# Kernel tuning notes

Measured on AMD Instinct MI355X. Metric: run time of the kernel, lower is better.

Reference implementation:

```python
import jax, jax.numpy as jnp
import numpy as np

NPOINT, RADIUS, NSAMPLE = 1024, 0.4, 32
BN_EPS = 1e-5


def fps(xyz, npoint):
    # xyz: [B, N, 3]. Deterministic start at index 0 (torch uses randint).
    B, N, _ = xyz.shape

    def step(carry, _):
        distance, farthest = carry  # [B,N], [B]
        centroid = jnp.take_along_axis(xyz, farthest[:, None, None], axis=1)  # [B,1,3]
        dist = jnp.sum((xyz - centroid) ** 2, -1)  # [B,N]
        distance = jnp.minimum(distance, dist)
        new_far = jnp.argmax(distance, axis=-1).astype(jnp.int32)
        return (distance, new_far), farthest

    init = (jnp.full((B, N), 1e10, xyz.dtype), jnp.zeros((B,), jnp.int32))
    _, cents = jax.lax.scan(step, init, None, length=npoint)  # [npoint, B]
    return cents.T  # [B, npoint]


def square_distance(src, dst):
    # src [B,S,3], dst [B,N,3] -> [B,S,N]
    d = -2.0 * jnp.einsum('bsc,bnc->bsn', src, dst)
    d = d + jnp.sum(src ** 2, -1)[:, :, None] + jnp.sum(dst ** 2, -1)[:, None, :]
    return jnp.clip(d, 1e-12, None)


def query_ball_point(radius, nsample, xyz, new_xyz):
    B, N, _ = xyz.shape
    S = new_xyz.shape[1]
    sqr = square_distance(new_xyz, xyz)  # [B,S,N]
    gi = jnp.where(sqr > radius ** 2, N, jnp.arange(N, dtype=jnp.int32)[None, None, :])
    gi = jnp.sort(gi, axis=-1)[:, :, :nsample]  # [B,S,K]
    first = gi[:, :, :1]
    return jnp.where(gi == N, first, gi)


def gather_points(points, idx):
    # points [B,N,C], idx [B,S,K] -> [B,S,K,C]
    B, S, K = idx.shape
    C = points.shape[-1]
    flat = jnp.take_along_axis(points, idx.reshape(B, S * K)[:, :, None], axis=1)
    return flat.reshape(B, S, K, C)


def setup_inputs() -> dict:
    key = jax.random.key(0)
    ks = jax.random.split(key, 10)
    B, N, D = 8, 4096, 64
    inp = {
        'xyz': jax.random.normal(ks[0], (B, 3, N), jnp.float32),
        'points': jax.random.normal(ks[1], (B, D, N), jnp.float32),
    }
    chans = [67, 64, 64, 128]
    for i in range(3):
        cin, cout = chans[i], chans[i + 1]
        inp[f'W{i}'] = jax.random.normal(ks[2 + i], (cout, cin), jnp.float32) * (1.0 / np.sqrt(cin))
        inp[f'b{i}'] = jnp.zeros((cout,), jnp.float32)
        inp[f'g{i}'] = jnp.ones((cout,), jnp.float32)
        inp[f'bt{i}'] = jnp.zeros((cout,), jnp.float32)
    return inp


def _forward(xyz, points, Ws, bs, gs, bts):
    xyz_t = jnp.transpose(xyz, (0, 2, 1))      # [B,N,3]
    pts_t = jnp.transpose(points, (0, 2, 1))   # [B,N,D]
    B, N, _ = xyz_t.shape

    fps_idx = fps(xyz_t, NPOINT)                              # [B,S]
    new_xyz = jnp.take_along_axis(xyz_t, fps_idx[:, :, None], axis=1)  # [B,S,3]
    idx = query_ball_point(RADIUS, NSAMPLE, xyz_t, new_xyz)   # [B,S,K]

    grouped_xyz = gather_points(xyz_t, idx)                   # [B,S,K,3]
    grouped_xyz_norm = grouped_xyz - new_xyz[:, :, None, :]
    grouped_pts = gather_points(pts_t, idx)                   # [B,S,K,D]
    new_points = jnp.concatenate([grouped_xyz_norm, grouped_pts], -1)  # [B,S,K,3+D]

    x = jnp.transpose(new_points, (0, 3, 2, 1))  # [B,C,K,S]
    for W, b, g, bt in zip(Ws, bs, gs, bts):
        x = jnp.einsum('oc,bcks->boks', W, x) + b[None, :, None, None]
        mean = jnp.mean(x, axis=(0, 2, 3), keepdims=True)
        var = jnp.var(x, axis=(0, 2, 3), keepdims=True)
        x = (x - mean) * jax.lax.rsqrt(var + BN_EPS)
        x = x * g[None, :, None, None] + bt[None, :, None, None]
        x = jax.nn.relu(x)
    out = jnp.max(x, axis=2)                      # [B,C_out,S]
    return jnp.transpose(new_xyz, (0, 2, 1)), out


def reference(xyz, points, W0, b0, g0, bt0, W1, b1, g1, bt1, W2, b2, g2, bt2):
    return _forward(xyz, points, (W0, W1, W2), (b0, b1, b2), (g0, g1, g2), (bt0, bt1, bt2))
```

## Files before the change

### kernel.cpp

```cpp
#include <hip/hip_runtime.h>
#include <cstddef>
#include <cstdint>

#define NB 8
#define NPTS 4096
#define NS 1024
#define NK 32
#define ND 64

typedef __attribute__((ext_vector_type(8))) short bf16x8;
typedef __attribute__((ext_vector_type(4))) float f32x4;

__device__ __forceinline__ short f2bf(float f) {
  unsigned u = __float_as_uint(f);
  u += 0x7FFF + ((u >> 16) & 1);
  return (short)(u >> 16);
}

#define DPP_IMAX(v, ctrl)                                                     \
  {                                                                           \
    int _o = __builtin_amdgcn_update_dpp(v, v, ctrl, 0xf, 0xf, false);        \
    v = (_o > v) ? _o : v;                                                    \
  }

#define DPP_U64MAX(hi, lo, ctrl)                                              \
  {                                                                           \
    unsigned _nh = (unsigned)__builtin_amdgcn_update_dpp((int)(hi), (int)(hi),\
                                                         ctrl, 0xf, 0xf, false);\
    unsigned _nl = (unsigned)__builtin_amdgcn_update_dpp((int)(lo), (int)(lo),\
                                                         ctrl, 0xf, 0xf, false);\
    bool _gt = (_nh > (hi)) || (_nh == (hi) && _nl > (lo));                   \
    hi = _gt ? _nh : (hi);                                                    \
    lo = _gt ? _nl : (lo);                                                    \
  }

#define DPP_FADD(v, ctrl)                                                     \
  {                                                                           \
    int _t = __builtin_amdgcn_update_dpp(__float_as_int(v), __float_as_int(v),\
                                         ctrl, 0xf, 0xf, false);              \
    v = v + __int_as_float(_t);                                               \
  }

#define DPP_RED16(v, OP)                                                      \
  {                                                                           \
    int _i;                                                                   \
    _i = __builtin_amdgcn_update_dpp(__float_as_int(v), __float_as_int(v), 0x111, 0xf, 0xf, false); \
    v = OP(v, __int_as_float(_i));                                            \
    _i = __builtin_amdgcn_update_dpp(__float_as_int(v), __float_as_int(v), 0x112, 0xf, 0xf, false); \
    v = OP(v, __int_as_float(_i));                                            \
    _i = __builtin_amdgcn_update_dpp(__float_as_int(v), __float_as_int(v), 0x114, 0xf, 0xf, false); \
    v = OP(v, __int_as_float(_i));                                            \
    _i = __builtin_amdgcn_update_dpp(__float_as_int(v), __float_as_int(v), 0x118, 0xf, 0xf, false); \
    v = OP(v, __int_as_float(_i));                                            \
  }

__device__ __forceinline__ float fadd_op(float a, float b) { return a + b; }

__global__ __launch_bounds__(512) void fps_pgemm_kernel(
    const float* __restrict__ xyz, float* __restrict__ out_newxyz,
    float* __restrict__ ws_newxyz, const float* __restrict__ points,
    const float* __restrict__ W0, const float* __restrict__ b0g,
    float* __restrict__ P1) {
  __shared__ __align__(16) char smem[53376];
  const int t = threadIdx.x;

  if (blockIdx.x < 8) {
    float* sXYZ = (float*)smem;
    unsigned long long(*sRed)[8] =
        (unsigned long long(*)[8])(smem + 49152);
    int* sWidx = (int*)(smem + 49280);
    const int b = blockIdx.x;
    const int wave = t >> 6;
    const int lane = t & 63;
    const float* xb = xyz + (size_t)b * 3 * NPTS;

    for (int i = t; i < NPTS; i += 512) {
      sXYZ[i * 3 + 0] = xb[i];
      sXYZ[i * 3 + 1] = xb[NPTS + i];
      sXYZ[i * 3 + 2] = xb[2 * NPTS + i];
    }
    if (t == 0) sWidx[0] = 0;

    float px[8], py[8], pz[8], dist[8];
    {
      float4 a0 = ((const float4*)xb)[2 * t];
      float4 a1 = ((const float4*)xb)[2 * t + 1];
      float4 b0v = ((const float4*)(xb + NPTS))[2 * t];
      float4 b1v = ((const float4*)(xb + NPTS))[2 * t + 1];
      float4 c0 = ((const float4*)(xb + 2 * NPTS))[2 * t];
      float4 c1 = ((const float4*)(xb + 2 * NPTS))[2 * t + 1];
      px[0] = a0.x; px[1] = a0.y; px[2] = a0.z; px[3] = a0.w;
      px[4] = a1.x; px[5] = a1.y; px[6] = a1.z; px[7] = a1.w;
      py[0] = b0v.x; py[1] = b0v.y; py[2] = b0v.z; py[3] = b0v.w;
      py[4] = b1v.x; py[5] = b1v.y; py[6] = b1v.z; py[7] = b1v.w;
      pz[0] = c0.x; pz[1] = c0.y; pz[2] = c0.z; pz[3] = c0.w;
      pz[4] = c1.x; pz[5] = c1.y; pz[6] = c1.z; pz[7] = c1.w;
    }
#pragma unroll
    for (int j = 0; j < 8; ++j) dist[j] = 1e10f;

    float cx = xb[0], cy = xb[NPTS], cz = xb[2 * NPTS];

    for (int s = 0; s < NS; ++s) {
#pragma unroll
      for (int j = 0; j < 8; ++j) {
        float dx = __fadd_rn(px[j], -cx);
        float dy = __fadd_rn(py[j], -cy);
        float dz = __fadd_rn(pz[j], -cz);
        float d = __fadd_rn(__fadd_rn(__fmul_rn(dx, dx), __fmul_rn(dy, dy)),
                            __fmul_rn(dz, dz));
        dist[j] = fminf(dist[j], d);
      }
      float m = fmaxf(fmaxf(fmaxf(dist[0], dist[1]), fmaxf(dist[2], dist[3])),
                      fmaxf(fmaxf(dist[4], dist[5]), fmaxf(dist[6], dist[7])));
      int v = __float_as_int(m);
      DPP_IMAX(v, 0x111)
      DPP_IMAX(v, 0x112)
      DPP_IMAX(v, 0x114)
      DPP_IMAX(v, 0x118)
      DPP_IMAX(v, 0x142)
      DPP_IMAX(v, 0x143)
      const int wm_i = __builtin_amdgcn_readlane(v, 63);
      const float wm = __int_as_float(wm_i);
      unsigned long long claim = __ballot(m == wm);
      int firstlane = __ffsll(claim) - 1;
      if (lane == firstlane) {
        int j = 7;
#pragma unroll
        for (int jj = 6; jj >= 0; --jj)
          if (dist[jj] == wm) j = jj;
        unsigned widx = (unsigned)(t * 8 + j);
        sRed[s & 1][wave] = ((unsigned long long)(unsigned)wm_i << 32) |
                            (unsigned long long)(0xFFFFFFFFu - widx);
      }
      __syncthreads();
      unsigned long long k = sRed[s & 1][lane & 7];
      unsigned h2 = (unsigned)(k >> 32), l2 = (unsigned)k;
      DPP_U64MAX(h2, l2, 0x111)
      DPP_U64MAX(h2, l2, 0x112)
      DPP_U64MAX(h2, l2, 0x114)
      const unsigned gl = (unsigned)__builtin_amdgcn_readlane((int)l2, 7);
      const int widx = (int)(0xFFFFFFFFu - gl);
      cx = sXYZ[widx * 3 + 0];
      cy = sXYZ[widx * 3 + 1];
      cz = sXYZ[widx * 3 + 2];
      if (t == 0 && s < NS - 1) sWidx[s + 1] = widx;
    }
    __syncthreads();
    for (int s2 = t; s2 < NS; s2 += 512) {
      int w = sWidx[s2];
      float x = sXYZ[w * 3 + 0], y = sXYZ[w * 3 + 1], z = sXYZ[w * 3 + 2];
      out_newxyz[b * 3 * NS + s2] = x;
      out_newxyz[b * 3 * NS + NS + s2] = y;
      out_newxyz[b * 3 * NS + 2 * NS + s2] = z;
      ws_newxyz[((b << 10) + s2) * 3 + 0] = x;
      ws_newxyz[((b << 10) + s2) * 3 + 1] = y;
      ws_newxyz[((b << 10) + s2) * 3 + 2] = z;
    }
  } else {
    float* sP = (float*)smem;
    float* sW = (float*)(smem + 16384);
    float* sB = (float*)(smem + 33792);
    const int blk = blockIdx.x - 8;
    const int bb = blk >> 6;
    const int n0 = (blk & 63) * 64;
    const float* pb = points + (size_t)bb * ND * NPTS;
    for (int f = t; f < 4096; f += 512) {
      int c = f >> 6, n = f & 63;
      sP[f] = pb[c * NPTS + n0 + n];
    }
    for (int f = t; f < 4096; f += 512) {
      int c = f >> 6, o = f & 63;
      sW[c * 68 + o] = W0[o * 67 + 3 + c];
    }
    if (t < 64) sB[t] = b0g[t];
    __syncthreads();
    if (t < 256) {
      const int nl = (t & 15) * 4;
      const int ol = (t >> 4) * 4;
      float acc[4][4];
#pragma unroll
      for (int i = 0; i < 4; ++i)
#pragma unroll
        for (int j = 0; j < 4; ++j) acc[i][j] = 0.f;
#pragma unroll 4
      for (int c = 0; c < 64; ++c) {
        float4 xv = *(const float4*)(sP + c * 64 + nl);
        float4 wv = *(const float4*)(sW + c * 68 + ol);
        float xa[4] = {xv.x, xv.y, xv.z, xv.w};
        float wa[4] = {wv.x, wv.y, wv.z, wv.w};
#pragma unroll
        for (int i = 0; i < 4; ++i)
#pragma unroll
          for (int j = 0; j < 4; ++j) acc[i][j] += xa[i] * wa[j];
      }
#pragma unroll
      for (int i = 0; i < 4; ++i) {
        float4 v = make_float4(acc[i][0] + sB[ol + 0], acc[i][1] + sB[ol + 1],
                               acc[i][2] + sB[ol + 2], acc[i][3] + sB[ol + 3]);
        *(float4*)(P1 + ((size_t)(bb << 12) + n0 + nl + i) * 64 + ol) = v;
      }
    }
  }
}

__global__ __launch_bounds__(256) void query_gstats_kernel(
    const float* __restrict__ xyz, const float* __restrict__ ws_newxyz,
    const float* __restrict__ P1, const float* __restrict__ W0,
    int* __restrict__ idx_ws, float* __restrict__ partials) {
  const int w = threadIdx.x >> 6;
  const int lane = threadIdx.x & 63;
  const int p = blockIdx.x * 4 + w;
  const int b = p >> 10;
  __shared__ int sIdx[4][32];
  __shared__ float sWS[4][64];
  __shared__ float sWQ[4][64];
  const float* xb = xyz + (size_t)b * 3 * NPTS;
  const float cx = ws_newxyz[p * 3 + 0];
  const float cy = ws_newxyz[p * 3 + 1];
  const float cz = ws_newxyz[p * 3 + 2];
  const float ss = __fadd_rn(__fadd_rn(__fmul_rn(cx, cx), __fmul_rn(cy, cy)), __fmul_rn(cz, cz));
  const float r2 = (float)(0.4 * 0.4);
  int cnt = 0;
  for (int ci = 0; ci < 64 && cnt < 32; ++ci) {
    int n = ci * 64 + lane;
    float x = xb[n], y = xb[NPTS + n], z = xb[2 * NPTS + n];
    float dot = __fadd_rn(__fadd_rn(__fmul_rn(cx, x), __fmul_rn(cy, y)), __fmul_rn(cz, z));
    float dd = __fadd_rn(__fadd_rn(__fmul_rn(x, x), __fmul_rn(y, y)), __fmul_rn(z, z));
    float d = __fmul_rn(-2.0f, dot);
    d = __fadd_rn(d, ss);
    d = __fadd_rn(d, dd);
    d = fmaxf(d, 1e-12f);
    bool inc = (d <= r2);
    unsigned long long m = __ballot(inc);
    int slot = cnt + (int)__popcll(m & ((1ull << lane) - 1ull));
    if (inc && slot < 32) sIdx[w][slot] = n;
    cnt += (int)__popcll(m);
  }
  if (lane < 32) {
    int v;
    if (lane < cnt) v = sIdx[w][lane];
    else v = (cnt > 0) ? sIdx[w][0] : 0;
    idx_ws[p * 32 + lane] = v;
    sIdx[w][lane] = v;
  }
  const float wx = W0[lane * 67 + 0];
  const float wy = W0[lane * 67 + 1];
  const float wz = W0[lane * 67 + 2];
  float ssum = 0.f, ssq = 0.f;
  for (int r = 0; r < 32; ++r) {
    const int n = sIdx[w][r];
    float P1v = P1[((size_t)(b << 12) + n) * 64 + lane];
    float dx = __fadd_rn(xb[n], -cx);
    float dy = __fadd_rn(xb[NPTS + n], -cy);
    float dz = __fadd_rn(xb[2 * NPTS + n], -cz);
    float y = P1v + (dx * wx + dy * wy + dz * wz);
    ssum += y;
    ssq += y * y;
  }
  sWS[w][lane] = ssum;
  sWQ[w][lane] = ssq;
  __syncthreads();
  const int t = threadIdx.x;
  if (t < 64) {
    float s1 = sWS[0][t] + sWS[1][t] + sWS[2][t] + sWS[3][t];
    float s2 = sWQ[0][t] + sWQ[1][t] + sWQ[2][t] + sWQ[3][t];
    partials[(size_t)blockIdx.x * 128 + t] = s1;
    partials[(size_t)blockIdx.x * 128 + 64 + t] = s2;
  }
}

__global__ __launch_bounds__(256) void conv1_kernel(
    const float* __restrict__ xyz, const float* __restrict__ P1,
    const int* __restrict__ idx_ws, const float* __restrict__ cen_ws,
    const float* __restrict__ W0, const float* __restrict__ W1,
    const float* __restrict__ bias, const float* __restrict__ scaleA,
    const float* __restrict__ shiftA, float* __restrict__ y1,
    float* __restrict__ partials) {
  constexpr int CIN = 64, COUT = 64, WP = 68, TPS = 128;
  __shared__ __align__(16) float sW[CIN * WP];
  __shared__ __align__(16) float sX[2 * CIN * 32];
  __shared__ float sY[64 * 65];
  __shared__ int sIdx[64];
  __shared__ float sCen[2 * 4];
  __shared__ float sScale[CIN];
  __shared__ float sShift[CIN];
  __shared__ float sSum[COUT];
  __shared__ float sSq[COUT];

  const int t = threadIdx.x;
  const int wave = t >> 6, lane = t & 63;
  const int pair0 = blockIdx.x * 2;
  const int b = pair0 >> 10;

  for (int f = t; f < CIN * COUT; f += 256) {
    int o = f / CIN;
    int c = f - o * CIN;
    sW[c * WP + o] = W1[f];
  }
  if (t < CIN) { sScale[t] = scaleA[t]; sShift[t] = shiftA[t]; }
  if (t < COUT) { sSum[t] = 0.f; sSq[t] = 0.f; }
  if (t < 64) sIdx[t] = idx_ws[pair0 * 32 + t];
  if (t < 6) sCen[(t / 3) * 4 + (t % 3)] = cen_ws[pair0 * 3 + t];
  const float wx = W0[lane * 67 + 0];
  const float wy = W0[lane * 67 + 1];
  const float wz = W0[lane * 67 + 2];
  __syncthreads();
  const float* xb = xyz + (size_t)b * 3 * NPTS;
  for (int r = wave; r < 64; r += 4) {
    const int sl = r >> 5;
    const int n = sIdx[r];
    float P1v = P1[((size_t)(b << 12) + n) * 64 + lane];
    float dx = __fadd_rn(xb[n], -sCen[sl * 4 + 0]);
    float dy = __fadd_rn(xb[NPTS + n], -sCen[sl * 4 + 1]);
    float dz = __fadd_rn(xb[2 * NPTS + n], -sCen[sl * 4 + 2]);
    sY[r * 65 + lane] = P1v + (dx * wx + dy * wy + dz * wz);
  }
  __syncthreads();
  for (int f = t; f < 2 * CIN * 32; f += 256) {
    int sl = f >> 11;
    int rmd = f & 2047;
    int o = rmd >> 5, k = rmd & 31;
    float v = sY[(sl * 32 + k) * 65 + o];
    v = v * sScale[o] + sShift[o];
    sX[f] = fmaxf(v, 0.f);
  }
  __syncthreads();

  const int sl = t / TPS;
  const int tl = t - sl * TPS;
  const int k0 = (tl & 7) * 4;
  const int o0 = (tl >> 3) * 4;

  float acc[4][4];
#pragma unroll
  for (int i = 0; i < 4; ++i)
#pragma unroll
    for (int j = 0; j < 4; ++j) acc[i][j] = 0.f;

  const float* xrow = sX + sl * (CIN * 32);
#pragma unroll 4
  for (int c = 0; c < CIN; ++c) {
    float4 xv = *(const float4*)(xrow + c * 32 + k0);
    float4 wv = *(const float4*)(sW + c * WP + o0);
    float xa[4] = {xv.x, xv.y, xv.z, xv.w};
    float wa[4] = {wv.x, wv.y, wv.z, wv.w};
#pragma unroll
    for (int i = 0; i < 4; ++i)
#pragma unroll
      for (int j = 0; j < 4; ++j) acc[i][j] += wa[i] * xa[j];
  }
#pragma unroll
  for (int i = 0; i < 4; ++i) {
    float bo = bias[o0 + i];
#pragma unroll
    for (int j = 0; j < 4; ++j) acc[i][j] += bo;
  }
#pragma unroll
  for (int i = 0; i < 4; ++i) {
    float s1 = (acc[i][0] + acc[i][1]) + (acc[i][2] + acc[i][3]);
    float s2 = (acc[i][0] * acc[i][0] + acc[i][1] * acc[i][1]) +
               (acc[i][2] * acc[i][2] + acc[i][3] * acc[i][3]);
    DPP_FADD(s1, 0x111)
    DPP_FADD(s1, 0x112)
    DPP_FADD(s1, 0x114)
    DPP_FADD(s2, 0x111)
    DPP_FADD(s2, 0x112)
    DPP_FADD(s2, 0x114)
    if ((t & 7) == 7) {
      atomicAdd(&sSum[o0 + i], s1);
      atomicAdd(&sSq[o0 + i], s2);
    }
  }
#pragma unroll
  for (int i = 0; i < 4; ++i) {
    float4 v = make_float4(acc[i][0], acc[i][1], acc[i][2], acc[i][3]);
    *(float4*)(y1 + (size_t)(pair0 + sl) * COUT * 32 + (o0 + i) * 32 + k0) = v;
  }
  __syncthreads();
  if (t < COUT) {
    partials[(size_t)blockIdx.x * (COUT * 2) + t] = sSum[t];
    partials[(size_t)blockIdx.x * (COUT * 2) + COUT + t] = sSq[t];
  }
}

__global__ __launch_bounds__(256) void conv2_mfma_kernel(
    const float* __restrict__ y1, const float* __restrict__ W2,
    const float* __restrict__ b2, const float* __restrict__ scaleA,
    const float* __restrict__ shiftA, float* __restrict__ pmax,
    float* __restrict__ pmin, float* __restrict__ partials) {
  __shared__ __align__(16) short sW2[128 * 72];
  __shared__ __align__(16) short sXb[32 * 72];
  __shared__ float sScale[64], sShift[64], sBias[128];
  __shared__ float sSum[128], sSq[128], sMax[128], sMin[128];

  const int t = threadIdx.x;
  const int s = blockIdx.x;
  const int lane = t & 63;
  const int wv = t >> 6;
  const int quad = lane >> 4;
  const int l15 = lane & 15;

  if (t < 64) { sScale[t] = scaleA[t]; sShift[t] = shiftA[t]; }
  if (t < 128) sBias[t] = b2[t];
  for (int f = t; f < 8192; f += 256) {
    int o = f >> 6, c = f & 63;
    sW2[o * 72 + c] = f2bf(W2[f]);
  }
  for (int f = t; f < 2048; f += 256) {
    int o = f >> 5, k = f & 31;
    float v = y1[(size_t)s * 2048 + f];
    v = v * sScale[o] + sShift[o];
    v = fmaxf(v, 0.f);
    sXb[k * 72 + o] = f2bf(v);
  }
  __syncthreads();

  f32x4 a00 = {0.f, 0.f, 0.f, 0.f}, a01 = {0.f, 0.f, 0.f, 0.f};
  f32x4 a10 = {0.f, 0.f, 0.f, 0.f}, a11 = {0.f, 0.f, 0.f, 0.f};
#pragma unroll
  for (int kh = 0; kh < 2; ++kh) {
    const int kc = kh * 32 + quad * 8;
    bf16x8 A0 = *(const bf16x8*)(sW2 + (wv * 32 + l15) * 72 + kc);
    bf16x8 A1 = *(const bf16x8*)(sW2 + (wv * 32 + 16 + l15) * 72 + kc);
    bf16x8 B0 = *(const bf16x8*)(sXb + l15 * 72 + kc);
    bf16x8 B1 = *(const bf16x8*)(sXb + (16 + l15) * 72 + kc);
    a00 = __builtin_amdgcn_mfma_f32_16x16x32_bf16(A0, B0, a00, 0, 0, 0);
    a01 = __builtin_amdgcn_mfma_f32_16x16x32_bf16(A0, B1, a01, 0, 0, 0);
    a10 = __builtin_amdgcn_mfma_f32_16x16x32_bf16(A1, B0, a10, 0, 0, 0);
    a11 = __builtin_amdgcn_mfma_f32_16x16x32_bf16(A1, B1, a11, 0, 0, 0);
  }

#pragma unroll
  for (int mi = 0; mi < 2; ++mi) {
    f32x4 L = mi ? a10 : a00;
    f32x4 R = mi ? a11 : a01;
    const int m0 = wv * 32 + mi * 16;
#pragma unroll
    for (int reg = 0; reg < 4; ++reg) {
      const int m = m0 + quad * 4 + reg;
      const float bb = sBias[m];
      float v0 = L[reg] + bb;
      float v1 = R[reg] + bb;
      float s1 = v0 + v1;
      float s2 = v0 * v0 + v1 * v1;
      float mx = fmaxf(v0, v1);
      float mn = fminf(v0, v1);
      DPP_RED16(s1, fadd_op)
      DPP_RED16(s2, fadd_op)
      DPP_RED16(mx, fmaxf)
      DPP_RED16(mn, fminf)
      if (l15 == 15) {
        sSum[m] = s1;
        sSq[m] = s2;
        sMax[m] = mx;
        sMin[m] = mn;
      }
    }
  }
  __syncthreads();
  if (t < 128) {
    partials[(size_t)s * 256 + t] = sSum[t];
    partials[(size_t)s * 256 + 128 + t] = sSq[t];
    pmax[(size_t)s * 128 + t] = sMax[t];
    pmin[(size_t)s * 128 + t] = sMin[t];
  }
}

template <int COUT>
__global__ __launch_bounds__(256) void stats_kernel(const float* __restrict__ partials,
                                                    int nblocks,
                                                    const float* __restrict__ gA,
                                                    const float* __restrict__ btA,
                                                    float* __restrict__ scaleA,
                                                    float* __restrict__ shiftA) {
  const int o = blockIdx.x;
  const int t = threadIdx.x;
  double s1 = 0.0, s2 = 0.0;
  for (int blk = t; blk < nblocks; blk += 256) {
    s1 += (double)partials[(size_t)blk * (COUT * 2) + o];
    s2 += (double)partials[(size_t)blk * (COUT * 2) + COUT + o];
  }
  __shared__ double r1[256], r2[256];
  r1[t] = s1; r2[t] = s2;
  __syncthreads();
  for (int st = 128; st > 0; st >>= 1) {
    if (t < st) { r1[t] += r1[t + st]; r2[t] += r2[t + st]; }
    __syncthreads();
  }
  if (t == 0) {
    const double Nr = 262144.0;
    double mean = r1[0] / Nr;
    double var = r2[0] / Nr - mean * mean;
    double rstd = 1.0 / sqrt(var + 1e-5);
    double sc = rstd * (double)gA[o];
    scaleA[o] = (float)sc;
    shiftA[o] = (float)((double)btA[o] - mean * sc);
  }
}

__global__ __launch_bounds__(256) void stats_final_kernel(
    const float* __restrict__ partials, int nblocks,
    const float* __restrict__ pmax, const float* __restrict__ pmin,
    const float* __restrict__ gA, const float* __restrict__ btA,
    float* __restrict__ out) {
  const int o = blockIdx.x;
  const int t = threadIdx.x;
  double s1 = 0.0, s2 = 0.0;
  for (int blk = t; blk < nblocks; blk += 256) {
    s1 += (double)partials[(size_t)blk * 256 + o];
    s2 += (double)partials[(size_t)blk * 256 + 128 + o];
  }
  __shared__ double r1[256], r2[256];
  __shared__ float sMean, sRstd;
  r1[t] = s1; r2[t] = s2;
  __syncthreads();
  for (int st = 128; st > 0; st >>= 1) {
    if (t < st) { r1[t] += r1[t + st]; r2[t] += r2[t + st]; }
    __syncthreads();
  }
  if (t == 0) {
    const double Nr = 262144.0;
    double mean = r1[0] / Nr;
    double var = r2[0] / Nr - mean * mean;
    sMean = (float)mean;
    sRstd = (float)(1.0 / sqrt(var + 1e-5));
  }
  __syncthreads();
  const float mn = sMean, rs = sRstd, gg = gA[o], bb = btA[o];
  const float slope = rs * gg;
  const float* src = (slope >= 0.f) ? pmax : pmin;
  for (int i = t; i < NB * NS; i += 256) {
    int b = i >> 10;
    int s = i & 1023;
    float v = src[(size_t)i * 128 + o];
    float t1 = (v - mn) * rs;
    float t2 = t1 * gg + bb;
    out[(size_t)b * (128 * NS) + o * NS + s] = fmaxf(t2, 0.f);
  }
}

extern "C" void kernel_launch(void* const* d_in, const int* in_sizes, int n_in,
                              void* d_out, int out_size, void* d_ws, size_t ws_size,
                              hipStream_t stream) {
  (void)in_sizes; (void)n_in; (void)out_size; (void)ws_size;
  const float* xyz = (const float*)d_in[0];
  const float* points = (const float*)d_in[1];
  const float* W0 = (const float*)d_in[2];
  const float* b0 = (const float*)d_in[3];
  const float* g0 = (const float*)d_in[4];
  const float* bt0 = (const float*)d_in[5];
  const float* W1 = (const float*)d_in[6];
  const float* b1 = (const float*)d_in[7];
  const float* g1 = (const float*)d_in[8];
  const float* bt1 = (const float*)d_in[9];
  const float* W2 = (const float*)d_in[10];
  const float* b2 = (const float*)d_in[11];
  const float* g2 = (const float*)d_in[12];
  const float* bt2 = (const float*)d_in[13];
  float* out = (float*)d_out;

  float* ws = (float*)d_ws;
  size_t off = 0;
  float* newxyz = ws + off;  off += (size_t)NB * NS * 3;
  int* idx = (int*)(ws + off); off += (size_t)NB * NS * NK;
  float* P1 = ws + off;      off += (size_t)NB * NPTS * 64;
  float* y1 = ws + off;      off += (size_t)NB * NS * 64 * 32;
  float* partials = ws + off; off += (size_t)8192 * 256;
  float* scaleA = ws + off;  off += 128;
  float* shiftA = ws + off;  off += 128;
  float* pmaxb = ws + off;   off += (size_t)NB * NS * 128;
  float* pminb = ws + off;   off += (size_t)NB * NS * 128;

  fps_pgemm_kernel<<<520, 512, 0, stream>>>(xyz, out, newxyz, points, W0, b0, P1);
  query_gstats_kernel<<<2048, 256, 0, stream>>>(xyz, newxyz, P1, W0, idx, partials);
  stats_kernel<64><<<64, 256, 0, stream>>>(partials, 2048, g0, bt0, scaleA, shiftA);
  conv1_kernel<<<4096, 256, 0, stream>>>(xyz, P1, idx, newxyz, W0, W1, b1,
                                         scaleA, shiftA, y1, partials);
  stats_kernel<64><<<64, 256, 0, stream>>>(partials, 4096, g1, bt1, scaleA, shiftA);
  conv2_mfma_kernel<<<8192, 256, 0, stream>>>(y1, W2, b2, scaleA, shiftA,
                                              pmaxb, pminb, partials);
  stats_final_kernel<<<128, 256, 0, stream>>>(partials, 8192, pmaxb, pminb,
                                              g2, bt2, out + NB * NS * 3);
}
```

Before: 1.009 ms.

## Move conv1 to bf16 MFMA and process two centroids per conv2 block

Replaces the scalar FP32 register-tiled conv1 GEMM with bf16 MFMA 16x16x32 instructions. BN0 and ReLU are now applied directly while staging the gathered inputs, which removes an intermediate shared buffer and a barrier. conv2 now handles two centroids per block, halving the grid and the number of partial-stat rows and reusing the bf16 W2 tile across more columns. The cost is bf16 rounding in conv1, which adds precision error before the batch-norm statistics.

```diff
diff --git a/kernel.cpp b/kernel.cpp
--- a/kernel.cpp
+++ b/kernel.cpp
@@ -270,117 +270,81 @@
   }
 }
 
-__global__ __launch_bounds__(256) void conv1_kernel(
+__global__ __launch_bounds__(256) void conv1_mfma_kernel(
     const float* __restrict__ xyz, const float* __restrict__ P1,
     const int* __restrict__ idx_ws, const float* __restrict__ cen_ws,
     const float* __restrict__ W0, const float* __restrict__ W1,
-    const float* __restrict__ bias, const float* __restrict__ scaleA,
+    const float* __restrict__ b1, const float* __restrict__ scaleA,
     const float* __restrict__ shiftA, float* __restrict__ y1,
     float* __restrict__ partials) {
-  constexpr int CIN = 64, COUT = 64, WP = 68, TPS = 128;
-  __shared__ __align__(16) float sW[CIN * WP];
-  __shared__ __align__(16) float sX[2 * CIN * 32];
-  __shared__ float sY[64 * 65];
+  __shared__ __align__(16) short sW1b[64 * 72];
+  __shared__ __align__(16) short sXb[64 * 72];
   __shared__ int sIdx[64];
   __shared__ float sCen[2 * 4];
-  __shared__ float sScale[CIN];
-  __shared__ float sShift[CIN];
-  __shared__ float sSum[COUT];
-  __shared__ float sSq[COUT];
+  __shared__ float sBias[64], sSum[64], sSq[64];
 
   const int t = threadIdx.x;
-  const int wave = t >> 6, lane = t & 63;
+  const int wv = t >> 6, lane = t & 63;
+  const int quad = lane >> 4, l15 = lane & 15;
   const int pair0 = blockIdx.x * 2;
   const int b = pair0 >> 10;
 
-  for (int f = t; f < CIN * COUT; f += 256) {
-    int o = f / CIN;
-    int c = f - o * CIN;
-    sW[c * WP + o] = W1[f];
-  }
-  if (t < CIN) { sScale[t] = scaleA[t]; sShift[t] = shiftA[t]; }
-  if (t < COUT) { sSum[t] = 0.f; sSq[t] = 0.f; }
-  if (t < 64) sIdx[t] = idx_ws[pair0 * 32 + t];
+  for (int f = t; f < 4096; f += 256) sW1b[(f >> 6) * 72 + (f & 63)] = f2bf(W1[f]);
+  if (t < 64) { sBias[t] = b1[t]; sIdx[t] = idx_ws[pair0 * 32 + t]; }
   if (t < 6) sCen[(t / 3) * 4 + (t % 3)] = cen_ws[pair0 * 3 + t];
   const float wx = W0[lane * 67 + 0];
   const float wy = W0[lane * 67 + 1];
   const float wz = W0[lane * 67 + 2];
+  const float sc = scaleA[lane];
+  const float sh = shiftA[lane];
   __syncthreads();
   const float* xb = xyz + (size_t)b * 3 * NPTS;
-  for (int r = wave; r < 64; r += 4) {
+  for (int r = wv; r < 64; r += 4) {
     const int sl = r >> 5;
     const int n = sIdx[r];
     float P1v = P1[((size_t)(b << 12) + n) * 64 + lane];
     float dx = __fadd_rn(xb[n], -sCen[sl * 4 + 0]);
     float dy = __fadd_rn(xb[NPTS + n], -sCen[sl * 4 + 1]);
     float dz = __fadd_rn(xb[2 * NPTS + n], -sCen[sl * 4 + 2]);
-    sY[r * 65 + lane] = P1v + (dx * wx + dy * wy + dz * wz);
-  }
-  __syncthreads();
-  for (int f = t; f < 2 * CIN * 32; f += 256) {
-    int sl = f >> 11;
-    int rmd = f & 2047;
-    int o = rmd >> 5, k = rmd & 31;
-    float v = sY[(sl * 32 + k) * 65 + o];
-    v = v * sScale[o] + sShift[o];
-    sX[f] = fmaxf(v, 0.f);
-  }
-  __syncthreads();
-
-  const int sl = t / TPS;
-  const int tl = t - sl * TPS;
-  const int k0 = (tl & 7) * 4;
-  const int o0 = (tl >> 3) * 4;
-
-  float acc[4][4];
-#pragma unroll
-  for (int i = 0; i < 4; ++i)
-#pragma unroll
-    for (int j = 0; j < 4; ++j) acc[i][j] = 0.f;
-
-  const float* xrow = sX + sl * (CIN * 32);
-#pragma unroll 4
-  for (int c = 0; c < CIN; ++c) {
-    float4 xv = *(const float4*)(xrow + c * 32 + k0);
-    float4 wv = *(const float4*)(sW + c * WP + o0);
-    float xa[4] = {xv.x, xv.y, xv.z, xv.w};
-    float wa[4] = {wv.x, wv.y, wv.z, wv.w};
-#pragma unroll
-    for (int i = 0; i < 4; ++i)
-#pragma unroll
-      for (int j = 0; j < 4; ++j) acc[i][j] += wa[i] * xa[j];
-  }
-#pragma unroll
-  for (int i = 0; i < 4; ++i) {
-    float bo = bias[o0 + i];
-#pragma unroll
-    for (int j = 0; j < 4; ++j) acc[i][j] += bo;
-  }
-#pragma unroll
-  for (int i = 0; i < 4; ++i) {
-    float s1 = (acc[i][0] + acc[i][1]) + (acc[i][2] + acc[i][3]);
-    float s2 = (acc[i][0] * acc[i][0] + acc[i][1] * acc[i][1]) +
-               (acc[i][2] * acc[i][2] + acc[i][3] * acc[i][3]);
-    DPP_FADD(s1, 0x111)
-    DPP_FADD(s1, 0x112)
-    DPP_FADD(s1, 0x114)
-    DPP_FADD(s2, 0x111)
-    DPP_FADD(s2, 0x112)
-    DPP_FADD(s2, 0x114)
-    if ((t & 7) == 7) {
-      atomicAdd(&sSum[o0 + i], s1);
-      atomicAdd(&sSq[o0 + i], s2);
-    }
-  }
-#pragma unroll
-  for (int i = 0; i < 4; ++i) {
-    float4 v = make_float4(acc[i][0], acc[i][1], acc[i][2], acc[i][3]);
-    *(float4*)(y1 + (size_t)(pair0 + sl) * COUT * 32 + (o0 + i) * 32 + k0) = v;
-  }
-  __syncthreads();
-  if (t < COUT) {
-    partials[(size_t)blockIdx.x * (COUT * 2) + t] = sSum[t];
-    partials[(size_t)blockIdx.x * (COUT * 2) + COUT + t] = sSq[t];
+    float y0 = P1v + (dx * wx + dy * wy + dz * wz);
+    sXb[r * 72 + lane] = f2bf(fmaxf(y0 * sc + sh, 0.f));
+  }
+  __syncthreads();
+
+  f32x4 acc[4];
+#pragma unroll
+  for (int i = 0; i < 4; ++i) acc[i] = (f32x4){0.f, 0.f, 0.f, 0.f};
+#pragma unroll
+  for (int kh = 0; kh < 2; ++kh) {
+    const int kc = kh * 32 + quad * 8;
+    bf16x8 A = *(const bf16x8*)(sW1b + (wv * 16 + l15) * 72 + kc);
+#pragma unroll
+    for (int ti = 0; ti < 4; ++ti) {
+      bf16x8 B = *(const bf16x8*)(sXb + (ti * 16 + l15) * 72 + kc);
+      acc[ti] = __builtin_amdgcn_mfma_f32_16x16x32_bf16(A, B, acc[ti], 0, 0, 0);
+    }
+  }
+
+#pragma unroll
+  for (int reg = 0; reg < 4; ++reg) {
+    const int m = wv * 16 + quad * 4 + reg;
+    const float bb = sBias[m];
+    float v[4];
+#pragma unroll
+    for (int ti = 0; ti < 4; ++ti) {
+      v[ti] = acc[ti][reg] + bb;
+      y1[(size_t)(pair0 + (ti >> 1)) * 2048 + m * 32 + (ti & 1) * 16 + l15] = v[ti];
+    }
+    float s1 = (v[0] + v[1]) + (v[2] + v[3]);
+    float s2 = (v[0] * v[0] + v[1] * v[1]) + (v[2] * v[2] + v[3] * v[3]);
+    DPP_RED16(s1, fadd_op)
+    DPP_RED16(s2, fadd_op)
+    if (l15 == 15) { sSum[m] = s1; sSq[m] = s2; }
+  }
+  __syncthreads();
+  if (t < 64) {
+    partials[(size_t)blockIdx.x * 128 + t] = sSum[t];
+    partials[(size_t)blockIdx.x * 128 + 64 + t] = sSq[t];
   }
 }
 
@@ -390,12 +354,13 @@
     const float* __restrict__ shiftA, float* __restrict__ pmax,
     float* __restrict__ pmin, float* __restrict__ partials) {
   __shared__ __align__(16) short sW2[128 * 72];
-  __shared__ __align__(16) short sXb[32 * 72];
+  __shared__ __align__(16) short sXb[64 * 72];
   __shared__ float sScale[64], sShift[64], sBias[128];
-  __shared__ float sSum[128], sSq[128], sMax[128], sMin[128];
+  __shared__ float sSum[128], sSq[128];
+  __shared__ float sMax[2][128], sMin[2][128];
 
   const int t = threadIdx.x;
-  const int s = blockIdx.x;
+  const int pair0 = blockIdx.x * 2;
   const int lane = t & 63;
   const int wv = t >> 6;
   const int quad = lane >> 4;
@@ -407,63 +372,73 @@
     int o = f >> 6, c = f & 63;
     sW2[o * 72 + c] = f2bf(W2[f]);
   }
-  for (int f = t; f < 2048; f += 256) {
-    int o = f >> 5, k = f & 31;
-    float v = y1[(size_t)s * 2048 + f];
+  for (int f = t; f < 4096; f += 256) {
+    int si = f >> 11;
+    int rmd = f & 2047;
+    int o = rmd >> 5, k = rmd & 31;
+    float v = y1[(size_t)(pair0 + si) * 2048 + rmd];
     v = v * sScale[o] + sShift[o];
     v = fmaxf(v, 0.f);
-    sXb[k * 72 + o] = f2bf(v);
-  }
-  __syncthreads();
-
-  f32x4 a00 = {0.f, 0.f, 0.f, 0.f}, a01 = {0.f, 0.f, 0.f, 0.f};
-  f32x4 a10 = {0.f, 0.f, 0.f, 0.f}, a11 = {0.f, 0.f, 0.f, 0.f};
+    sXb[(si * 32 + k) * 72 + o] = f2bf(v);
+  }
+  __syncthreads();
+
+  f32x4 acc[2][4];
+#pragma unroll
+  for (int i = 0; i < 2; ++i)
+#pragma unroll
+    for (int ti = 0; ti < 4; ++ti) acc[i][ti] = (f32x4){0.f, 0.f, 0.f, 0.f};
 #pragma unroll
   for (int kh = 0; kh < 2; ++kh) {
     const int kc = kh * 32 + quad * 8;
     bf16x8 A0 = *(const bf16x8*)(sW2 + (wv * 32 + l15) * 72 + kc);
     bf16x8 A1 = *(const bf16x8*)(sW2 + (wv * 32 + 16 + l15) * 72 + kc);
-    bf16x8 B0 = *(const bf16x8*)(sXb + l15 * 72 + kc);
-    bf16x8 B1 = *(const bf16x8*)(sXb + (16 + l15) * 72 + kc);
-    a00 = __builtin_amdgcn_mfma_f32_16x16x32_bf16(A0, B0, a00, 0, 0, 0);
-    a01 = __builtin_amdgcn_mfma_f32_16x16x32_bf16(A0, B1, a01, 0, 0, 0);
-    a10 = __builtin_amdgcn_mfma_f32_16x16x32_bf16(A1, B0, a10, 0, 0, 0);
-    a11 = __builtin_amdgcn_mfma_f32_16x16x32_bf16(A1, B1, a11, 0, 0, 0);
-  }
-
-#pragma unroll
-  for (int mi = 0; mi < 2; ++mi) {
-    f32x4 L = mi ? a10 : a00;
-    f32x4 R = mi ? a11 : a01;
-    const int m0 = wv * 32 + mi * 16;
+#pragma unroll
+    for (int ti = 0; ti < 4; ++ti) {
+      bf16x8 B = *(const bf16x8*)(sXb + (ti * 16 + l15) * 72 + kc);
+      acc[0][ti] = __builtin_amdgcn_mfma_f32_16x16x32_bf16(A0, B, acc[0][ti], 0, 0, 0);
+      acc[1][ti] = __builtin_amdgcn_mfma_f32_16x16x32_bf16(A1, B, acc[1][ti], 0, 0, 0);
+    }
+  }
+
+#pragma unroll
+  for (int i = 0; i < 2; ++i) {
 #pragma unroll
     for (int reg = 0; reg < 4; ++reg) {
-      const int m = m0 + quad * 4 + reg;
+      const int m = wv * 32 + i * 16 + quad * 4 + reg;
       const float bb = sBias[m];
-      float v0 = L[reg] + bb;
-      float v1 = R[reg] + bb;
-      float s1 = v0 + v1;
-      float s2 = v0 * v0 + v1 * v1;
-      float mx = fmaxf(v0, v1);
-      float mn = fminf(v0, v1);
+      float v0 = acc[i][0][reg] + bb;
+      float v1 = acc[i][1][reg] + bb;
+      float v2 = acc[i][2][reg] + bb;
+      float v3 = acc[i][3][reg] + bb;
+      float s1 = (v0 + v1) + (v2 + v3);
+      float s2 = (v0 * v0 + v1 * v1) + (v2 * v2 + v3 * v3);
+      float mx0 = fmaxf(v0, v1), mn0 = fminf(v0, v1);
+      float mx1 = fmaxf(v2, v3), mn1 = fminf(v2, v3);
       DPP_RED16(s1, fadd_op)
       DPP_RED16(s2, fadd_op)
-      DPP_RED16(mx, fmaxf)
-      DPP_RED16(mn, fminf)
+      DPP_RED16(mx0, fmaxf)
+      DPP_RED16(mn0, fminf)
+      DPP_RED16(mx1, fmaxf)
+      DPP_RED16(mn1, fminf)
       if (l15 == 15) {
         sSum[m] = s1;
         sSq[m] = s2;
-        sMax[m] = mx;
-        sMin[m] = mn;
+        sMax[0][m] = mx0;
+        sMin[0][m] = mn0;
+        sMax[1][m] = mx1;
+        sMin[1][m] = mn1;
       }
     }
   }
   __syncthreads();
   if (t < 128) {
-    partials[(size_t)s * 256 + t] = sSum[t];
-    partials[(size_t)s * 256 + 128 + t] = sSq[t];
-    pmax[(size_t)s * 128 + t] = sMax[t];
-    pmin[(size_t)s * 128 + t] = sMin[t];
+    partials[(size_t)blockIdx.x * 256 + t] = sSum[t];
+    partials[(size_t)blockIdx.x * 256 + 128 + t] = sSq[t];
+    pmax[(size_t)pair0 * 128 + t] = sMax[0][t];
+    pmin[(size_t)pair0 * 128 + t] = sMin[0][t];
+    pmax[(size_t)(pair0 + 1) * 128 + t] = sMax[1][t];
+    pmin[(size_t)(pair0 + 1) * 128 + t] = sMin[1][t];
   }
 }
 
@@ -575,11 +550,11 @@
   fps_pgemm_kernel<<<520, 512, 0, stream>>>(xyz, out, newxyz, points, W0, b0, P1);
   query_gstats_kernel<<<2048, 256, 0, stream>>>(xyz, newxyz, P1, W0, idx, partials);
   stats_kernel<64><<<64, 256, 0, stream>>>(partials, 2048, g0, bt0, scaleA, shiftA);
-  conv1_kernel<<<4096, 256, 0, stream>>>(xyz, P1, idx, newxyz, W0, W1, b1,
-                                         scaleA, shiftA, y1, partials);
+  conv1_mfma_kernel<<<4096, 256, 0, stream>>>(xyz, P1, idx, newxyz, W0, W1, b1,
+                                              scaleA, shiftA, y1, partials);
   stats_kernel<64><<<64, 256, 0, stream>>>(partials, 4096, g1, bt1, scaleA, shiftA);
-  conv2_mfma_kernel<<<8192, 256, 0, stream>>>(y1, W2, b2, scaleA, shiftA,
+  conv2_mfma_kernel<<<4096, 256, 0, stream>>>(y1, W2, b2, scaleA, shiftA,
                                               pmaxb, pminb, partials);
-  stats_final_kernel<<<128, 256, 0, stream>>>(partials, 8192, pmaxb, pminb,
+  stats_final_kernel<<<128, 256, 0, stream>>>(partials, 4096, pmaxb, pminb,
                                               g2, bt2, out + NB * NS * 3);
 }
```

After: 969.2 us. 3.9% less time.
